# Optimization experiments

Hardware: AMD Instinct MI355X
Metric: run time of the kernel (lower is better)

Reference implementation:

```python
import jax, jax.numpy as jnp
import numpy as np

T, D = 32768, 768
NS = NQ = 8192
L = 6


def setup_inputs() -> dict:
    key = jax.random.key(0)
    ks = jax.random.split(key, 8)
    return {
        "tok_support": jax.random.normal(ks[0], (T, D), dtype=jnp.float32),
        "tok_query": jax.random.normal(ks[1], (T, D), dtype=jnp.float32),
        "start_s": jax.random.randint(ks[2], (NS,), 0, T),
        "end_s": jax.random.randint(ks[3], (NS,), 0, T),
        "start_q": jax.random.randint(ks[4], (NQ,), 0, T),
        "end_q": jax.random.randint(ks[5], (NQ,), 0, T),
        "labels_s": jax.random.randint(ks[6], (NS,), 0, L),
        "num_labels": L,
    }


def reference(tok_support, tok_query, start_s, end_s, start_q, end_q, labels_s, num_labels):
    # Span embeddings: concat(start token emb, end token emb)  -> [N, 2D]
    S = jnp.concatenate([tok_support[start_s], tok_support[end_s]], axis=-1)  # [NS, 2D]
    Q = jnp.concatenate([tok_query[start_q], tok_query[end_q]], axis=-1)      # [NQ, 2D]
    # dist[q, s] = -||Q_q - S_s||^2 = 2 Q.S - ||Q||^2 - ||S||^2 (same math, no [NQ,NS,2D] temp)
    dist = (2.0 * (Q @ S.T)
            - jnp.sum(Q * Q, axis=-1, keepdims=True)
            - jnp.sum(S * S, axis=-1)[None, :])  # [NQ, NS]
    NEG = jnp.finfo(dist.dtype).min
    # per-label nearest (max) support distance; num_labels is a small fixed int
    logits = jnp.stack(
        [jnp.max(jnp.where(labels_s == l, dist, NEG), axis=1) for l in range(num_labels)],
        axis=1,
    )  # [NQ, num_labels]
    pred = jnp.argmax(logits, axis=1)
    return logits, pred
```

## Files before the change

### kernel.cpp

```cpp
#include <hip/hip_runtime.h>

#define D_TOK 768
#define NS 8192
#define NQ 8192
#define NL 6
#define KDIM 1536
#define BM 256
#define BN 256
#define NTN 32
#define NITER 12

typedef __attribute__((ext_vector_type(4))) float f32x4;
typedef __attribute__((ext_vector_type(8))) short bf16x8;
typedef unsigned int u32;
typedef unsigned short u16;

__device__ __forceinline__ u16 f2bf(float f) {
    u32 u = __float_as_uint(f);
    u32 r = (u + 0x7FFFu + ((u >> 16) & 1u)) >> 16;
    return (u16)r;
}

__global__ __launch_bounds__(256) void prep_kernel(
    const float* __restrict__ tok_support, const float* __restrict__ tok_query,
    const int* __restrict__ start_s, const int* __restrict__ end_s,
    const int* __restrict__ start_q, const int* __restrict__ end_q,
    u16* __restrict__ Qb, u16* __restrict__ Sb,
    float* __restrict__ qn, float* __restrict__ sn) {
    int gw = (blockIdx.x * 256 + threadIdx.x) >> 6;
    int lane = threadIdx.x & 63;
    const float* tok;
    const int *st, *en;
    u16* dst;
    float* nrm;
    int r;
    if (gw < NQ) {
        r = gw; tok = tok_query; st = start_q; en = end_q;
        dst = Qb + (size_t)r * KDIM; nrm = qn + r;
    } else {
        r = gw - NQ; tok = tok_support; st = start_s; en = end_s;
        dst = Sb + (size_t)r * KDIM; nrm = sn + r;
    }
    float ssum = 0.0f;
#pragma unroll
    for (int h = 0; h < 2; ++h) {
        const float4* src4 =
            (const float4*)(tok + (size_t)(h ? en[r] : st[r]) * D_TOK);
        u16* d = dst + h * D_TOK;
#pragma unroll
        for (int it = 0; it < 3; ++it) {
            int i = lane + it * 64;
            float4 v = src4[i];
            ssum += v.x * v.x + v.y * v.y + v.z * v.z + v.w * v.w;
            ushort4 b;
            b.x = f2bf(v.x); b.y = f2bf(v.y); b.z = f2bf(v.z); b.w = f2bf(v.w);
            ((ushort4*)d)[i] = b;
        }
    }
#pragma unroll
    for (int s = 32; s; s >>= 1) ssum += __shfl_xor(ssum, s);
    if (lane == 0) *nrm = ssum;
}

__global__ __launch_bounds__(512) void gemm_kernel(
    const u16* __restrict__ Qb, const u16* __restrict__ Sb,
    const float* __restrict__ qn, const float* __restrict__ sn,
    const int* __restrict__ labels, float* __restrict__ part) {
    __shared__ char lds[131072];
    u16* As = (u16*)lds;
    u16* Bs = (u16*)(lds + 65536);
    const char* Ab = (const char*)lds;
    const char* Bb = (const char*)(lds + 65536);

    const int tid = threadIdx.x;
    const int lane = tid & 63;
    const int wid = tid >> 6;
    const int wm = wid >> 2;
    const int wn = wid & 3;
    const int l15 = lane & 15;
    const int lq = lane >> 4;

    const int bid = blockIdx.x;
    const int x = bid & 7;
    const int lid = bid >> 3;
    const int tm = x * 4 + (lid & 3);
    const int tn = lid >> 2;
    const int bm = tm * BM;
    const int bn = tn * BN;

    int grow[4], gcol[4];
#pragma unroll
    for (int j = 0; j < 4; ++j) {
        int p = j * 8192 + tid * 16;
        int q = p ^ (((p >> 9) & 1) << 5);
        grow[j] = q >> 7;
        gcol[j] = (q & 127) >> 1;
    }
    const u16* gA = Qb + (size_t)bm * KDIM;
    const u16* gB = Sb + (size_t)bn * KDIM;

    const int swz = ((l15 >> 2) & 1) << 5;
    const int aBase = ((wm * 128 + l15) * 128 + lq * 16) ^ swz;
    const int bBase = ((wn * 64 + l15) * 128 + lq * 16) ^ swz;

    f32x4 acc[8][4] = {};
    bf16x8 af[4][2], bf[2][2];

#define STG(dst, g, b, t)                                                     \
    do {                                                                      \
        _Pragma("unroll") for (int j = 0; j < 4; ++j) {                       \
            __builtin_amdgcn_global_load_lds(                                 \
                (__attribute__((address_space(1))) void*)(u16*)(              \
                    (g) + (size_t)grow[j] * KDIM + (t) * 64 + gcol[j]),       \
                (__attribute__((address_space(3))) void*)(                    \
                    (dst) + (b) * 16384 + j * 4096 + tid * 8),                \
                16, 0, 0);                                                    \
        }                                                                     \
    } while (0)

#define READ_A(b, m0)                                                         \
    do {                                                                      \
        _Pragma("unroll") for (int i = 0; i < 4; ++i)                         \
            _Pragma("unroll") for (int kk = 0; kk < 2; ++kk)                  \
                af[i][kk] = *(const bf16x8*)(Ab + (b) * 32768 + aBase +       \
                                             ((m0) + i) * 2048 + kk * 64);    \
    } while (0)

#define READ_B(b, n0)                                                         \
    do {                                                                      \
        _Pragma("unroll") for (int jj = 0; jj < 2; ++jj)                      \
            _Pragma("unroll") for (int kk = 0; kk < 2; ++kk)                  \
                bf[jj][kk] = *(const bf16x8*)(Bb + (b) * 32768 + bBase +      \
                                              ((n0) + jj) * 2048 + kk * 64);  \
    } while (0)

#define MFMA_Q(m0, n0)                                                        \
    do {                                                                      \
        __builtin_amdgcn_s_setprio(1);                                        \
        _Pragma("unroll") for (int i = 0; i < 4; ++i)                         \
            _Pragma("unroll") for (int jj = 0; jj < 2; ++jj)                  \
                _Pragma("unroll") for (int kk = 0; kk < 2; ++kk)              \
                    acc[(m0) + i][(n0) + jj] =                                \
                        __builtin_amdgcn_mfma_f32_16x16x32_bf16(              \
                            af[i][kk], bf[jj][kk], acc[(m0) + i][(n0) + jj],  \
                            0, 0, 0);                                         \
        __builtin_amdgcn_s_setprio(0);                                        \
    } while (0)

#define BAR __builtin_amdgcn_s_barrier()
#define HANDOFF(N)                                                            \
    do {                                                                      \
        __builtin_amdgcn_sched_barrier(0);                                    \
        asm volatile("s_waitcnt vmcnt(" #N ")" ::: "memory");                 \
        __builtin_amdgcn_s_barrier();                                         \
        __builtin_amdgcn_sched_barrier(0);                                    \
    } while (0)

    STG(As, gA, 0, 0);
    STG(Bs, gB, 0, 0);
    STG(As, gA, 1, 1);
    HANDOFF(4);

#pragma unroll 1
    for (int it = 0; it < NITER; ++it) {
        const int more = (it < NITER - 1);
        READ_A(0, 0);
        READ_B(0, 0);
        STG(Bs, gB, 1, 2 * it + 1);
        BAR;
        MFMA_Q(0, 0);
        BAR;
        READ_B(0, 2);
        BAR;
        MFMA_Q(0, 2);
        BAR;
        READ_A(0, 4);
        READ_B(0, 0);
        BAR;
        MFMA_Q(4, 0);
        BAR;
        READ_B(0, 2);
        if (more) STG(As, gA, 0, 2 * it + 2);
        BAR;
        MFMA_Q(4, 2);
        if (more) { HANDOFF(4); } else { HANDOFF(0); }
        READ_A(1, 0);
        READ_B(1, 0);
        if (more) STG(Bs, gB, 0, 2 * it + 2);
        BAR;
        MFMA_Q(0, 0);
        BAR;
        READ_B(1, 2);
        BAR;
        MFMA_Q(0, 2);
        BAR;
        READ_A(1, 4);
        READ_B(1, 0);
        BAR;
        MFMA_Q(4, 0);
        BAR;
        READ_B(1, 2);
        if (more) STG(As, gA, 1, 2 * it + 3);
        BAR;
        MFMA_Q(4, 2);
        if (more) { HANDOFF(4); } else { HANDOFF(0); }
    }

    float* red = (float*)lds;
    const float NEGF = -3.402823466e38f;
    float sncol[4];
    int lab[4];
#pragma unroll
    for (int n = 0; n < 4; ++n) {
        int c = bn + wn * 64 + n * 16 + l15;
        sncol[n] = sn[c];
        lab[n] = labels[c];
    }
#pragma unroll
    for (int m = 0; m < 8; ++m) {
#pragma unroll
        for (int j = 0; j < 4; ++j) {
            int rl = m * 16 + lq * 4 + j;
            float q2 = qn[bm + wm * 128 + rl];
            float lmax[NL];
#pragma unroll
            for (int t = 0; t < NL; ++t) lmax[t] = NEGF;
#pragma unroll
            for (int n = 0; n < 4; ++n) {
                float v = 2.0f * acc[m][n][j] - q2 - sncol[n];
#pragma unroll
                for (int t = 0; t < NL; ++t)
                    lmax[t] = fmaxf(lmax[t], lab[n] == t ? v : NEGF);
            }
#pragma unroll
            for (int t = 0; t < NL; ++t) {
                float v = lmax[t];
                v = fmaxf(v, __shfl_xor(v, 1));
                v = fmaxf(v, __shfl_xor(v, 2));
                v = fmaxf(v, __shfl_xor(v, 4));
                v = fmaxf(v, __shfl_xor(v, 8));
                if (l15 == t)
                    red[((wm * 128 + rl) * 4 + wn) * NL + t] = v;
            }
        }
    }
    __syncthreads();
    for (int i = tid; i < 256 * NL; i += 512) {
        int rf = i / NL, t = i - rf * NL;
        float v = fmaxf(
            fmaxf(red[(rf * 4 + 0) * NL + t], red[(rf * 4 + 1) * NL + t]),
            fmaxf(red[(rf * 4 + 2) * NL + t], red[(rf * 4 + 3) * NL + t]));
        part[(size_t)(bm + rf) * (NTN * NL) + tn * NL + t] = v;
    }
#undef STG
#undef READ_A
#undef READ_B
#undef MFMA_Q
#undef BAR
#undef HANDOFF
}

__global__ __launch_bounds__(256) void final_kernel(
    const float* __restrict__ part, float* __restrict__ out) {
    int q = (blockIdx.x * 256 + threadIdx.x) >> 6;
    int lane = threadIdx.x & 63;
    const float NEGF = -3.402823466e38f;
    float v[NL];
    if (lane < NTN) {
        const float* p = part + ((size_t)q * NTN + lane) * NL;
#pragma unroll
        for (int t = 0; t < NL; ++t) v[t] = p[t];
    } else {
#pragma unroll
        for (int t = 0; t < NL; ++t) v[t] = NEGF;
    }
#pragma unroll
    for (int t = 0; t < NL; ++t) {
#pragma unroll
        for (int s = 32; s; s >>= 1) v[t] = fmaxf(v[t], __shfl_xor(v[t], s));
    }
    if (lane == 0) {
        float best = NEGF;
        int bi = 0;
#pragma unroll
        for (int t = 0; t < NL; ++t) {
            out[q * NL + t] = v[t];
            if (v[t] > best) { best = v[t]; bi = t; }
        }
        out[NQ * NL + q] = (float)bi;
    }
}

extern "C" void kernel_launch(void* const* d_in, const int* in_sizes, int n_in,
                              void* d_out, int out_size, void* d_ws,
                              size_t ws_size, hipStream_t stream) {
    const float* tok_support = (const float*)d_in[0];
    const float* tok_query = (const float*)d_in[1];
    const int* start_s = (const int*)d_in[2];
    const int* end_s = (const int*)d_in[3];
    const int* start_q = (const int*)d_in[4];
    const int* end_q = (const int*)d_in[5];
    const int* labels_s = (const int*)d_in[6];

    char* ws = (char*)d_ws;
    u16* Qb = (u16*)ws;
    u16* Sb = (u16*)(ws + 25165824);
    float* qn = (float*)(ws + 50331648);
    float* sn = (float*)(ws + 50364416);
    float* part = (float*)(ws + 50397184);

    prep_kernel<<<dim3((NQ + NS) / 4), dim3(256), 0, stream>>>(
        tok_support, tok_query, start_s, end_s, start_q, end_q, Qb, Sb, qn, sn);
    gemm_kernel<<<dim3(32 * 32), dim3(512), 0, stream>>>(Qb, Sb, qn, sn,
                                                         labels_s, part);
    final_kernel<<<dim3(NQ * 64 / 256), dim3(256), 0, stream>>>(part,
                                                                (float*)d_out);
}
```

Measured before the change: 543.5 us.

## Restructure GEMM main loop: hold full B fragments, stream A in pairs, XOR-8 swizzle

The main loop now loads all four B fragments per wave once per K-step and streams A in two-row pairs, issuing 8 MFMAs per phase. Global-to-LDS staging is split into half-chunks interleaved across phases, and the LDS layout uses a full 8-way XOR swizzle in place of the single-bit swizzle. The block-to-tile mapping is changed so tiles are swept along M within a column group, and a syncthreads is added before the LDS is reused for the reduction. The aim is fewer redundant B LDS reads, fewer bank conflicts and smoother load/compute overlap. The cost is more registers held for B fragments and a different cache-reuse pattern across blocks.

```diff
diff --git a/kernel.cpp b/kernel.cpp
--- a/kernel.cpp
+++ b/kernel.cpp
@@ -83,67 +83,66 @@
     const int bid = blockIdx.x;
     const int x = bid & 7;
     const int lid = bid >> 3;
-    const int tm = x * 4 + (lid & 3);
-    const int tn = lid >> 2;
+    const int tn = x * 4 + (lid >> 5);
+    const int tm = lid & 31;
     const int bm = tm * BM;
     const int bn = tn * BN;
 
-    int grow[4], gcol[4];
-#pragma unroll
-    for (int j = 0; j < 4; ++j) {
-        int p = j * 8192 + tid * 16;
-        int q = p ^ (((p >> 9) & 1) << 5);
-        grow[j] = q >> 7;
-        gcol[j] = (q & 127) >> 1;
-    }
+    const int growb = tid >> 3;
+    const int gcol = ((tid & 7) ^ (growb & 7)) * 8;
     const u16* gA = Qb + (size_t)bm * KDIM;
     const u16* gB = Sb + (size_t)bn * KDIM;
 
-    const int swz = ((l15 >> 2) & 1) << 5;
-    const int aBase = ((wm * 128 + l15) * 128 + lq * 16) ^ swz;
-    const int bBase = ((wn * 64 + l15) * 128 + lq * 16) ^ swz;
+    const int xr = l15 & 7;
+    const int oK0 = (lq ^ xr) * 16;
+    const int oK1 = ((lq + 4) ^ xr) * 16;
+    const int aRow = (wm * 128 + l15) * 128;
+    const int bRow = (wn * 64 + l15) * 128;
 
     f32x4 acc[8][4] = {};
-    bf16x8 af[4][2], bf[2][2];
-
-#define STG(dst, g, b, t)                                                     \
-    do {                                                                      \
-        _Pragma("unroll") for (int j = 0; j < 4; ++j) {                       \
+    bf16x8 af[2][2], bfr[4][2];
+
+#define STG2(dstU16, g, bsel, j0_, t)                                         \
+    do {                                                                      \
+        _Pragma("unroll") for (int j = (j0_); j < (j0_) + 2; ++j) {           \
             __builtin_amdgcn_global_load_lds(                                 \
                 (__attribute__((address_space(1))) void*)(u16*)(              \
-                    (g) + (size_t)grow[j] * KDIM + (t) * 64 + gcol[j]),       \
+                    (g) + (size_t)(j * 64 + growb) * KDIM +                   \
+                    (size_t)(t) * 64 + gcol),                                 \
                 (__attribute__((address_space(3))) void*)(                    \
-                    (dst) + (b) * 16384 + j * 4096 + tid * 8),                \
+                    (dstU16) + (bsel) * 16384 + j * 4096 + tid * 8),          \
                 16, 0, 0);                                                    \
         }                                                                     \
     } while (0)
 
-#define READ_A(b, m0)                                                         \
-    do {                                                                      \
-        _Pragma("unroll") for (int i = 0; i < 4; ++i)                         \
+#define READ_A2(bsel, m0)                                                     \
+    do {                                                                      \
+        _Pragma("unroll") for (int i = 0; i < 2; ++i)                         \
             _Pragma("unroll") for (int kk = 0; kk < 2; ++kk)                  \
-                af[i][kk] = *(const bf16x8*)(Ab + (b) * 32768 + aBase +       \
-                                             ((m0) + i) * 2048 + kk * 64);    \
-    } while (0)
-
-#define READ_B(b, n0)                                                         \
-    do {                                                                      \
-        _Pragma("unroll") for (int jj = 0; jj < 2; ++jj)                      \
+                af[i][kk] = *(const bf16x8*)(Ab + (bsel) * 32768 + aRow +     \
+                                             ((m0) + i) * 2048 +              \
+                                             (kk ? oK1 : oK0));               \
+    } while (0)
+
+#define READ_BALL(bsel)                                                       \
+    do {                                                                      \
+        _Pragma("unroll") for (int n = 0; n < 4; ++n)                         \
             _Pragma("unroll") for (int kk = 0; kk < 2; ++kk)                  \
-                bf[jj][kk] = *(const bf16x8*)(Bb + (b) * 32768 + bBase +      \
-                                              ((n0) + jj) * 2048 + kk * 64);  \
-    } while (0)
-
-#define MFMA_Q(m0, n0)                                                        \
-    do {                                                                      \
+                bfr[n][kk] = *(const bf16x8*)(Bb + (bsel) * 32768 + bRow +    \
+                                              n * 2048 + (kk ? oK1 : oK0));   \
+    } while (0)
+
+#define MFMA_P(m0)                                                            \
+    do {                                                                      \
+        __builtin_amdgcn_sched_barrier(0);                                    \
         __builtin_amdgcn_s_setprio(1);                                        \
-        _Pragma("unroll") for (int i = 0; i < 4; ++i)                         \
-            _Pragma("unroll") for (int jj = 0; jj < 2; ++jj)                  \
+        _Pragma("unroll") for (int i = 0; i < 2; ++i)                         \
+            _Pragma("unroll") for (int n = 0; n < 4; ++n)                     \
                 _Pragma("unroll") for (int kk = 0; kk < 2; ++kk)              \
-                    acc[(m0) + i][(n0) + jj] =                                \
+                    acc[(m0) + i][n] =                                        \
                         __builtin_amdgcn_mfma_f32_16x16x32_bf16(              \
-                            af[i][kk], bf[jj][kk], acc[(m0) + i][(n0) + jj],  \
-                            0, 0, 0);                                         \
+                            af[i][kk], bfr[n][kk], acc[(m0) + i][n], 0, 0,    \
+                            0);                                               \
         __builtin_amdgcn_s_setprio(0);                                        \
     } while (0)
 
@@ -156,55 +155,43 @@
         __builtin_amdgcn_sched_barrier(0);                                    \
     } while (0)
 
-    STG(As, gA, 0, 0);
-    STG(Bs, gB, 0, 0);
-    STG(As, gA, 1, 1);
+    STG2(As, gA, 0, 0, 0); STG2(As, gA, 0, 2, 0);
+    STG2(Bs, gB, 0, 0, 0); STG2(Bs, gB, 0, 2, 0);
+    STG2(Bs, gB, 1, 0, 1); STG2(Bs, gB, 1, 2, 1);
     HANDOFF(4);
 
 #pragma unroll 1
     for (int it = 0; it < NITER; ++it) {
         const int more = (it < NITER - 1);
-        READ_A(0, 0);
-        READ_B(0, 0);
-        STG(Bs, gB, 1, 2 * it + 1);
-        BAR;
-        MFMA_Q(0, 0);
-        BAR;
-        READ_B(0, 2);
-        BAR;
-        MFMA_Q(0, 2);
-        BAR;
-        READ_A(0, 4);
-        READ_B(0, 0);
-        BAR;
-        MFMA_Q(4, 0);
-        BAR;
-        READ_B(0, 2);
-        if (more) STG(As, gA, 0, 2 * it + 2);
-        BAR;
-        MFMA_Q(4, 2);
+        const int t1 = 2 * it + 1, t2 = 2 * it + 2, t3 = 2 * it + 3;
+        READ_BALL(0); READ_A2(0, 0);
+        STG2(As, gA, 1, 0, t1);
+        BAR; MFMA_P(0); BAR;
+        READ_A2(0, 2);
+        STG2(As, gA, 1, 2, t1);
+        BAR; MFMA_P(2); BAR;
+        READ_A2(0, 4);
+        if (more) STG2(Bs, gB, 0, 0, t2);
+        BAR; MFMA_P(4); BAR;
+        READ_A2(0, 6);
+        if (more) STG2(Bs, gB, 0, 2, t2);
+        BAR; MFMA_P(6);
         if (more) { HANDOFF(4); } else { HANDOFF(0); }
-        READ_A(1, 0);
-        READ_B(1, 0);
-        if (more) STG(Bs, gB, 0, 2 * it + 2);
-        BAR;
-        MFMA_Q(0, 0);
-        BAR;
-        READ_B(1, 2);
-        BAR;
-        MFMA_Q(0, 2);
-        BAR;
-        READ_A(1, 4);
-        READ_B(1, 0);
-        BAR;
-        MFMA_Q(4, 0);
-        BAR;
-        READ_B(1, 2);
-        if (more) STG(As, gA, 1, 2 * it + 3);
-        BAR;
-        MFMA_Q(4, 2);
+        READ_BALL(1); READ_A2(1, 0);
+        if (more) STG2(As, gA, 0, 0, t2);
+        BAR; MFMA_P(0); BAR;
+        READ_A2(1, 2);
+        if (more) STG2(As, gA, 0, 2, t2);
+        BAR; MFMA_P(2); BAR;
+        READ_A2(1, 4);
+        if (more) STG2(Bs, gB, 1, 0, t3);
+        BAR; MFMA_P(4); BAR;
+        READ_A2(1, 6);
+        if (more) STG2(Bs, gB, 1, 2, t3);
+        BAR; MFMA_P(6);
         if (more) { HANDOFF(4); } else { HANDOFF(0); }
     }
+    __syncthreads();
 
     float* red = (float*)lds;
     const float NEGF = -3.402823466e38f;
@@ -252,10 +239,10 @@
             fmaxf(red[(rf * 4 + 2) * NL + t], red[(rf * 4 + 3) * NL + t]));
         part[(size_t)(bm + rf) * (NTN * NL) + tn * NL + t] = v;
     }
-#undef STG
-#undef READ_A
-#undef READ_B
-#undef MFMA_Q
+#undef STG2
+#undef READ_A2
+#undef READ_BALL
+#undef MFMA_P
 #undef BAR
 #undef HANDOFF
 }
```

After: 512.3 us. 5.7% less time.
